# Optimization experiments

Measured on AMD Instinct MI355X. Metric: run time of the kernel, lower is better.

## Reference

```python
import jax, jax.numpy as jnp
import numpy as np

B, L, D_MODEL = 2, 4096, 256
D_STATE, D_CONV, EXPAND = 16, 4, 2
D_INNER = EXPAND * D_MODEL
DT_RANK = D_MODEL // 16
D_FF = 2048


def setup_inputs() -> dict:
    key = jax.random.key(0)
    ks = jax.random.split(key, 14)
    s = 0.02
    A_log = jnp.log(jnp.tile(jnp.arange(1, D_STATE + 1, dtype=jnp.float32), (D_INNER, 1)))
    return {
        "x": jax.random.normal(ks[0], (B, L, D_MODEL), jnp.float32),
        "in_proj_w": jax.random.normal(ks[1], (2 * D_INNER, D_MODEL), jnp.float32) * s,
        "conv_w": jax.random.normal(ks[2], (D_INNER, D_CONV), jnp.float32) * s,
        "conv_b": jax.random.normal(ks[3], (D_INNER,), jnp.float32) * s,
        "x_proj_w": jax.random.normal(ks[4], (DT_RANK + 2 * D_STATE, D_INNER), jnp.float32) * s,
        "dt_proj_w": jax.random.normal(ks[5], (D_INNER, DT_RANK), jnp.float32) * s,
        "dt_proj_b": jax.random.uniform(ks[6], (D_INNER,), jnp.float32, -4.0, -2.0),
        "A_log": A_log,
        "D": jnp.ones((D_INNER,), jnp.float32),
        "out_proj_w": jax.random.normal(ks[7], (D_MODEL, D_INNER), jnp.float32) * s,
        "lin1_w": jax.random.normal(ks[8], (D_FF, D_MODEL), jnp.float32) * s,
        "lin1_b": jnp.zeros((D_FF,), jnp.float32),
        "lin2_w": jax.random.normal(ks[9], (D_FF, D_FF), jnp.float32) * s,
        "lin2_b": jnp.zeros((D_FF,), jnp.float32),
    }


def reference(x, in_proj_w, conv_w, conv_b, x_proj_w, dt_proj_w, dt_proj_b,
              A_log, D, out_proj_w, lin1_w, lin1_b, lin2_w, lin2_b):
    b, l, _ = x.shape
    d_inner = conv_w.shape[0]
    d_state = A_log.shape[1]
    dt_rank = dt_proj_w.shape[1]
    d_conv = conv_w.shape[1]

    # in_proj -> split into x and gate z
    xz = x @ in_proj_w.T                       # (B,L,2*Din)
    xin, z = jnp.split(xz, 2, axis=-1)

    # causal depthwise conv1d + SiLU
    xc = jnp.transpose(xin, (0, 2, 1))         # (B,Din,L)
    xc = jax.lax.conv_general_dilated(
        xc, conv_w[:, None, :], (1,), [(d_conv - 1, 0)],
        dimension_numbers=("NCH", "OIH", "NCH"), feature_group_count=d_inner)
    xc = xc + conv_b[None, :, None]
    u = jax.nn.silu(jnp.transpose(xc, (0, 2, 1)))  # (B,L,Din)

    # input-dependent SSM params
    x_dbl = u @ x_proj_w.T                     # (B,L,dt_rank+2*N)
    dt, Bt, Ct = jnp.split(x_dbl, [dt_rank, dt_rank + d_state], axis=-1)
    delta = jax.nn.softplus(dt @ dt_proj_w.T + dt_proj_b)  # (B,L,Din)

    A = -jnp.exp(A_log)                        # (Din,N)
    dA = jnp.exp(delta[..., None] * A)         # (B,L,Din,N)
    dBu = delta[..., None] * Bt[:, :, None, :] * u[..., None]  # (B,L,Din,N)

    def step(h, inp):
        dA_t, dBu_t, C_t = inp
        h = dA_t * h + dBu_t                   # (B,Din,N)
        y = jnp.einsum("bdn,bn->bd", h, C_t)
        return h, y

    h0 = jnp.zeros((b, d_inner, d_state), x.dtype)
    _, ys = jax.lax.scan(step, h0, (jnp.swapaxes(dA, 0, 1),
                                    jnp.swapaxes(dBu, 0, 1),
                                    jnp.swapaxes(Ct, 0, 1)))
    y = jnp.swapaxes(ys, 0, 1) + u * D         # (B,L,Din)
    y = y * jax.nn.silu(z)
    m = y @ out_proj_w.T                       # (B,L,d_model)

    # trailing MLP: lin2(relu(lin1(.)))
    h1 = jax.nn.relu(m @ lin1_w.T + lin1_b)
    return h1 @ lin2_w.T + lin2_b
```

## Files before the change

kernel.cpp:

```cpp
#include <hip/hip_runtime.h>
#include <hip/hip_bf16.h>
#include <stdint.h>

#define BB  2
#define LL  4096
#define DM  256
#define DI  512
#define NST 16
#define DTR 16
#define DFF 2048
#define ML  (BB*LL)

#define NCHUNK 128
#define CHUNK  32
#define BDN    (BB*DI*NST)

typedef __attribute__((ext_vector_type(8))) short s16x8;
typedef __attribute__((ext_vector_type(4))) float f32x4;

__device__ __forceinline__ ushort f2bf(float f) {
  union { float f; uint32_t u; } v; v.f = f;
  return (ushort)((v.u + 0x7FFFu + ((v.u >> 16) & 1u)) >> 16);
}

__device__ __forceinline__ void async16(const void* g, void* l) {
  __builtin_amdgcn_global_load_lds(
      (const __attribute__((address_space(1))) void*)g,
      (__attribute__((address_space(3))) void*)l, 16, 0, 0);
}

__global__ void k_f2b(const float* __restrict__ src, ushort* __restrict__ dst, int n4) {
  int i = blockIdx.x * 256 + threadIdx.x;
  if (i >= n4) return;
  f32x4 v = ((const f32x4*)src)[i];
  *(ushort4*)&dst[i * 4] = make_ushort4(f2bf(v[0]), f2bf(v[1]), f2bf(v[2]), f2bf(v[3]));
}

__global__ void k_xprojw(const float* __restrict__ src, ushort* __restrict__ dst) {
  int i = blockIdx.x * 256 + threadIdx.x;
  if (i >= 128 * DI / 4) return;
  int e = i * 4;
  int r = e >> 9;
  int c = e & 511;
  ushort4 o;
  if (r < DTR + 2 * NST) {
    f32x4 v = *(const f32x4*)&src[r * DI + c];
    o = make_ushort4(f2bf(v[0]), f2bf(v[1]), f2bf(v[2]), f2bf(v[3]));
  } else {
    o = make_ushort4(0, 0, 0, 0);
  }
  *(ushort4*)&dst[e] = o;
}

template<int OUTF, int OUTB, int BIAS, int RELU>
__global__ __launch_bounds__(256)
void k_gemm(const ushort* __restrict__ A, const ushort* __restrict__ W,
            const float* __restrict__ bias,
            float* __restrict__ outF, ushort* __restrict__ outB,
            int M, int N, int K) {
  __shared__ __align__(16) ushort AsB[3][128 * 32];
  __shared__ __align__(16) ushort BsB[3][128 * 32];
  const int tid  = threadIdx.x;
  const int lane = tid & 63;
  const int wv   = tid >> 6;

  const int nwg  = gridDim.x * gridDim.y;
  const int flat = blockIdx.y * gridDim.x + blockIdx.x;
  const int cpx  = nwg >> 3;
  const int swz  = (flat & 7) * cpx + (flat >> 3);
  const int m0 = (swz / gridDim.x) << 7;
  const int n0 = (swz % gridDim.x) << 7;

  const int wr = (wv >> 1) << 6;
  const int wc = (wv & 1) << 6;
  const int lr = lane & 15;
  const int hi = lane >> 4;

  f32x4 acc[4][4] = {};

  const int sr0 = (wv << 5) + (lane >> 2);
  const int sc  = lane & 3;

  const int nt = K >> 5;

  auto STAGE = [&](int t, int bi) {
    const int k0 = t << 5;
#pragma unroll
    for (int j = 0; j < 2; ++j) {
      const int r  = sr0 + j * 16;
      const int cs = sc ^ ((r >> 1) & 3);
      async16(A + (size_t)(m0 + r) * K + k0 + cs * 8, &AsB[bi][((wv << 5) + j * 16) * 32]);
      async16(W + (size_t)(n0 + r) * K + k0 + cs * 8, &BsB[bi][((wv << 5) + j * 16) * 32]);
    }
  };

  STAGE(0, 0);
  STAGE(1, 1);

  int cur = 0;
  for (int t = 0; t < nt; ++t) {
    if (t + 1 < nt) { asm volatile("s_waitcnt vmcnt(4)" ::: "memory"); }
    else            { asm volatile("s_waitcnt vmcnt(0)" ::: "memory"); }
    __builtin_amdgcn_s_barrier();
    __builtin_amdgcn_sched_barrier(0);

    if (t + 2 < nt) {
      int nx2 = cur + 2; if (nx2 >= 3) nx2 -= 3;
      STAGE(t + 2, nx2);
    }

    const ushort* As = AsB[cur];
    const ushort* Bs = BsB[cur];
    s16x8 af[4], bf_[4];
#pragma unroll
    for (int mi = 0; mi < 4; ++mi) {
      const int row = wr + mi * 16 + lr;
      af[mi] = *(const s16x8*)&As[row * 32 + ((hi ^ ((row >> 1) & 3)) << 3)];
    }
#pragma unroll
    for (int ni = 0; ni < 4; ++ni) {
      const int row = wc + ni * 16 + lr;
      bf_[ni] = *(const s16x8*)&Bs[row * 32 + ((hi ^ ((row >> 1) & 3)) << 3)];
    }
    asm volatile("s_waitcnt lgkmcnt(0)" ::: "memory");
    __builtin_amdgcn_sched_barrier(0);

    __builtin_amdgcn_s_setprio(1);
#pragma unroll
    for (int mi = 0; mi < 4; ++mi)
#pragma unroll
      for (int ni = 0; ni < 4; ++ni)
        acc[mi][ni] = __builtin_amdgcn_mfma_f32_16x16x32_bf16(af[mi], bf_[ni], acc[mi][ni], 0, 0, 0);
    __builtin_amdgcn_s_setprio(0);

    cur = (cur + 1 == 3) ? 0 : cur + 1;
  }

#pragma unroll
  for (int mi = 0; mi < 4; ++mi) {
#pragma unroll
    for (int ni = 0; ni < 4; ++ni) {
      const int gc = n0 + wc + ni * 16 + lr;
      const float b = BIAS ? bias[gc] : 0.f;
#pragma unroll
      for (int i = 0; i < 4; ++i) {
        const int gr = m0 + wr + mi * 16 + (hi << 2) + i;
        float v = acc[mi][ni][i] + b;
        if (RELU) v = fmaxf(v, 0.f);
        if (OUTF) outF[(size_t)gr * N + gc] = v;
        if (OUTB) outB[(size_t)gr * N + gc] = f2bf(v);
      }
    }
  }
}

__global__ void k_conv(const float* __restrict__ xz, const float* __restrict__ cw,
                       const float* __restrict__ cb,
                       float* __restrict__ u, ushort* __restrict__ u_bf) {
  const int i = blockIdx.x * 256 + threadIdx.x;
  if (i >= ML * DI / 4) return;
  const int d4 = i & (DI / 4 - 1);
  const int bl = i / (DI / 4);
  const int l  = bl & (LL - 1);
  const int d  = d4 << 2;
  f32x4 acc;
  acc[0] = cb[d]; acc[1] = cb[d + 1]; acc[2] = cb[d + 2]; acc[3] = cb[d + 3];
#pragma unroll
  for (int j = 0; j < 4; ++j) {
    const int lj = l - 3 + j;
    if (lj >= 0) {
      const f32x4 xv = *(const f32x4*)&xz[(size_t)(bl + j - 3) * 1024 + d];
      acc[0] += xv[0] * cw[(d + 0) * 4 + j];
      acc[1] += xv[1] * cw[(d + 1) * 4 + j];
      acc[2] += xv[2] * cw[(d + 2) * 4 + j];
      acc[3] += xv[3] * cw[(d + 3) * 4 + j];
    }
  }
  f32x4 o;
#pragma unroll
  for (int c = 0; c < 4; ++c) o[c] = acc[c] / (1.f + __expf(-acc[c]));
  *(f32x4*)&u[(size_t)bl * DI + d] = o;
  *(ushort4*)&u_bf[(size_t)bl * DI + d] =
      make_ushort4(f2bf(o[0]), f2bf(o[1]), f2bf(o[2]), f2bf(o[3]));
}

__global__ __launch_bounds__(256)
void k_scan1(const float* __restrict__ u, const float* __restrict__ xdbl,
             const float* __restrict__ A_log, const float* __restrict__ dtw,
             const float* __restrict__ dtb,
             float* __restrict__ Pw, float* __restrict__ Sw) {
  const int c = blockIdx.x;
  const int b = blockIdx.y >> 1;
  const int d = ((blockIdx.y & 1) << 8) + threadIdx.x;
  __shared__ float sdt[CHUNK][16], sB[CHUNK][16];
  {
    const int i = threadIdx.x * 2;
    const int t = i >> 4, n = i & 15;
    const size_t g = ((size_t)b * LL + (size_t)c * CHUNK + t) * 128 + n;
    *(float2*)&sdt[t][n] = *(const float2*)&xdbl[g];
    *(float2*)&sB[t][n]  = *(const float2*)&xdbl[g + DTR];
  }
  float An[16], wreg[16];
#pragma unroll
  for (int j = 0; j < 4; ++j) {
    f32x4 a = *(const f32x4*)&A_log[d * 16 + j * 4];
    f32x4 w = *(const f32x4*)&dtw[d * 16 + j * 4];
#pragma unroll
    for (int q = 0; q < 4; ++q) { An[j * 4 + q] = -__expf(a[q]); wreg[j * 4 + q] = w[q]; }
  }
  const float bd = dtb[d];
  float P[16], S[16];
#pragma unroll
  for (int n = 0; n < 16; ++n) { P[n] = 1.f; S[n] = 0.f; }
  __syncthreads();

  const size_t rowbase = ((size_t)b * LL + (size_t)c * CHUNK) * DI + d;
  float ut = u[rowbase];
  for (int t = 0; t < CHUNK; ++t) {
    const float ut_n = (t + 1 < CHUNK) ? u[rowbase + (size_t)(t + 1) * DI] : 0.f;
    float a = bd;
#pragma unroll
    for (int k2 = 0; k2 < 16; ++k2) a = fmaf(sdt[t][k2], wreg[k2], a);
    const float dt = (a > 15.f) ? a : log1pf(__expf(a));
    const float k = dt * ut;
#pragma unroll
    for (int n = 0; n < 16; ++n) {
      const float dA = __expf(dt * An[n]);
      S[n] = fmaf(dA, S[n], k * sB[t][n]);
      P[n] *= dA;
    }
    ut = ut_n;
  }
  float* Pp = Pw + ((size_t)c * BDN) + ((size_t)b * DI + d) * 16;
  float* Sp = Sw + ((size_t)c * BDN) + ((size_t)b * DI + d) * 16;
#pragma unroll
  for (int j = 0; j < 4; ++j) {
    f32x4 pv, sv;
#pragma unroll
    for (int q = 0; q < 4; ++q) { pv[q] = P[j * 4 + q]; sv[q] = S[j * 4 + q]; }
    *(f32x4*)&Pp[j * 4] = pv;
    *(f32x4*)&Sp[j * 4] = sv;
  }
}

__global__ void k_scan2(float* __restrict__ Pw, const float* __restrict__ Sw) {
  const int f = blockIdx.x * 256 + threadIdx.x;
  float h = 0.f;
#pragma unroll 4
  for (int c = 0; c < NCHUNK; ++c) {
    const float Pc = Pw[(size_t)c * BDN + f];
    const float Sc = Sw[(size_t)c * BDN + f];
    Pw[(size_t)c * BDN + f] = h;
    h = fmaf(Pc, h, Sc);
  }
}

__global__ __launch_bounds__(256)
void k_scan3(const float* __restrict__ u, const float* __restrict__ xdbl,
             const float* __restrict__ xz, const float* __restrict__ A_log,
             const float* __restrict__ dtw, const float* __restrict__ dtb,
             const float* __restrict__ Dp,
             const float* __restrict__ Hs, ushort* __restrict__ y_bf) {
  const int c = blockIdx.x;
  const int b = blockIdx.y >> 1;
  const int d = ((blockIdx.y & 1) << 8) + threadIdx.x;
  __shared__ float sdt[CHUNK][16], sB[CHUNK][16], sC[CHUNK][16];
  {
    const int i = threadIdx.x * 2;
    const int t = i >> 4, n = i & 15;
    const size_t g = ((size_t)b * LL + (size_t)c * CHUNK + t) * 128 + n;
    *(float2*)&sdt[t][n] = *(const float2*)&xdbl[g];
    *(float2*)&sB[t][n]  = *(const float2*)&xdbl[g + DTR];
    *(float2*)&sC[t][n]  = *(const float2*)&xdbl[g + DTR + NST];
  }
  float An[16], wreg[16];
#pragma unroll
  for (int j = 0; j < 4; ++j) {
    f32x4 a = *(const f32x4*)&A_log[d * 16 + j * 4];
    f32x4 w = *(const f32x4*)&dtw[d * 16 + j * 4];
#pragma unroll
    for (int q = 0; q < 4; ++q) { An[j * 4 + q] = -__expf(a[q]); wreg[j * 4 + q] = w[q]; }
  }
  const float bd = dtb[d];
  float h[16];
  {
    const float* Hp = Hs + ((size_t)c * BDN) + ((size_t)b * DI + d) * 16;
#pragma unroll
    for (int j = 0; j < 4; ++j) {
      f32x4 v = *(const f32x4*)&Hp[j * 4];
#pragma unroll
      for (int q = 0; q < 4; ++q) h[j * 4 + q] = v[q];
    }
  }
  const float Dd = Dp[d];
  __syncthreads();

  const size_t rowbase = ((size_t)b * LL + (size_t)c * CHUNK) * DI + d;
  const size_t zbase   = ((size_t)b * LL + (size_t)c * CHUNK) * 1024 + DI + d;
  float ut = u[rowbase];
  float zt = xz[zbase];
  for (int t = 0; t < CHUNK; ++t) {
    float ut_n = 0.f, zt_n = 0.f;
    if (t + 1 < CHUNK) {
      ut_n = u[rowbase + (size_t)(t + 1) * DI];
      zt_n = xz[zbase + (size_t)(t + 1) * 1024];
    }
    float a = bd;
#pragma unroll
    for (int k2 = 0; k2 < 16; ++k2) a = fmaf(sdt[t][k2], wreg[k2], a);
    const float dt = (a > 15.f) ? a : log1pf(__expf(a));
    const float k = dt * ut;
    float y = 0.f;
#pragma unroll
    for (int n = 0; n < 16; ++n) {
      const float dA = __expf(dt * An[n]);
      h[n] = fmaf(dA, h[n], k * sB[t][n]);
      y = fmaf(h[n], sC[t][n], y);
    }
    y = (y + ut * Dd) * (zt / (1.f + __expf(-zt)));
    y_bf[rowbase + (size_t)t * DI] = f2bf(y);
    ut = ut_n; zt = zt_n;
  }
}

extern "C" void kernel_launch(void* const* d_in, const int* in_sizes, int n_in,
                              void* d_out, int out_size, void* d_ws, size_t ws_size,
                              hipStream_t stream) {
  const float* x          = (const float*)d_in[0];
  const float* in_proj_w  = (const float*)d_in[1];
  const float* conv_w     = (const float*)d_in[2];
  const float* conv_b     = (const float*)d_in[3];
  const float* x_proj_w   = (const float*)d_in[4];
  const float* dt_proj_w  = (const float*)d_in[5];
  const float* dt_proj_b  = (const float*)d_in[6];
  const float* A_log      = (const float*)d_in[7];
  const float* Dp         = (const float*)d_in[8];
  const float* out_proj_w = (const float*)d_in[9];
  const float* lin1_w     = (const float*)d_in[10];
  const float* lin1_b     = (const float*)d_in[11];
  const float* lin2_w     = (const float*)d_in[12];
  const float* lin2_b     = (const float*)d_in[13];
  float* out = (float*)d_out;

  char* p = (char*)d_ws;
  auto carve = [&](size_t bytes) -> char* {
    char* r = p;
    p += (bytes + 255) & ~(size_t)255;
    return r;
  };
  ushort* x_bf   = (ushort*)carve((size_t)ML * DM * 2);
  ushort* wip_bf = (ushort*)carve((size_t)2 * DI * DM * 2);
  float*  xz     = (float*) carve((size_t)ML * 1024 * 4);
  float*  u      = (float*) carve((size_t)ML * DI * 4);
  ushort* u_bf   = (ushort*)carve((size_t)ML * DI * 2);
  ushort* xpw_bf = (ushort*)carve((size_t)128 * DI * 2);
  float*  xdbl   = (float*) carve((size_t)ML * 128 * 4);
  ushort* y_bf   = (ushort*)carve((size_t)ML * DI * 2);
  ushort* opw_bf = (ushort*)carve((size_t)DM * DI * 2);
  ushort* l1w_bf = (ushort*)carve((size_t)DFF * DM * 2);
  float*  Pws    = (float*) carve((size_t)NCHUNK * BDN * 4);
  float*  Sws    = (float*) carve((size_t)NCHUNK * BDN * 4);
  ushort* m_bf   = u_bf;
  ushort* h1_bf  = (ushort*)xz;
  ushort* l2w_bf = (ushort*)u;

  k_f2b<<<(ML * DM / 4 + 255) / 256, 256, 0, stream>>>(x, x_bf, ML * DM / 4);
  k_f2b<<<(2 * DI * DM / 4 + 255) / 256, 256, 0, stream>>>(in_proj_w, wip_bf, 2 * DI * DM / 4);
  k_gemm<1, 0, 0, 0><<<dim3(1024 / 128, ML / 128), 256, 0, stream>>>(
      x_bf, wip_bf, nullptr, xz, nullptr, ML, 1024, DM);
  k_conv<<<(ML * DI / 4 + 255) / 256, 256, 0, stream>>>(xz, conv_w, conv_b, u, u_bf);
  k_xprojw<<<(128 * DI / 4 + 255) / 256, 256, 0, stream>>>(x_proj_w, xpw_bf);
  k_gemm<1, 0, 0, 0><<<dim3(1, ML / 128), 256, 0, stream>>>(
      u_bf, xpw_bf, nullptr, xdbl, nullptr, ML, 128, DI);
  k_scan1<<<dim3(NCHUNK, BB * 2), 256, 0, stream>>>(u, xdbl, A_log, dt_proj_w,
                                                    dt_proj_b, Pws, Sws);
  k_scan2<<<BDN / 256, 256, 0, stream>>>(Pws, Sws);
  k_scan3<<<dim3(NCHUNK, BB * 2), 256, 0, stream>>>(u, xdbl, xz, A_log, dt_proj_w,
                                                    dt_proj_b, Dp, Pws, y_bf);
  k_f2b<<<(DM * DI / 4 + 255) / 256, 256, 0, stream>>>(out_proj_w, opw_bf, DM * DI / 4);
  k_gemm<0, 1, 0, 0><<<dim3(DM / 128, ML / 128), 256, 0, stream>>>(
      y_bf, opw_bf, nullptr, nullptr, m_bf, ML, DM, DI);
  k_f2b<<<(DFF * DM / 4 + 255) / 256, 256, 0, stream>>>(lin1_w, l1w_bf, DFF * DM / 4);
  k_gemm<0, 1, 1, 1><<<dim3(DFF / 128, ML / 128), 256, 0, stream>>>(
      m_bf, l1w_bf, lin1_b, nullptr, h1_bf, ML, DFF, DM);
  k_f2b<<<(DFF * DFF / 4 + 255) / 256, 256, 0, stream>>>(lin2_w, l2w_bf, DFF * DFF / 4);
  k_gemm<1, 0, 1, 0><<<dim3(DFF / 128, ML / 128), 256, 0, stream>>>(
      h1_bf, l2w_bf, lin2_b, out, nullptr, ML, DFF, DFF);
}
```

Baseline: 378.3 us.

## Add 256x256-tile 8-wave GEMM with 4-stage pipeline for MLP layers

```diff
diff --git a/kernel.cpp b/kernel.cpp
--- a/kernel.cpp
+++ b/kernel.cpp
@@ -67,7 +67,7 @@
   const int nwg  = gridDim.x * gridDim.y;
   const int flat = blockIdx.y * gridDim.x + blockIdx.x;
   const int cpx  = nwg >> 3;
-  const int swz  = (flat & 7) * cpx + (flat >> 3);
+  const int swz  = (nwg & 7) ? flat : (flat & 7) * cpx + (flat >> 3);
   const int m0 = (swz / gridDim.x) << 7;
   const int n0 = (swz % gridDim.x) << 7;
 
@@ -80,7 +80,6 @@
 
   const int sr0 = (wv << 5) + (lane >> 2);
   const int sc  = lane & 3;
-
   const int nt = K >> 5;
 
   auto STAGE = [&](int t, int bi) {
@@ -145,6 +144,107 @@
 #pragma unroll
       for (int i = 0; i < 4; ++i) {
         const int gr = m0 + wr + mi * 16 + (hi << 2) + i;
+        float v = acc[mi][ni][i] + b;
+        if (RELU) v = fmaxf(v, 0.f);
+        if (OUTF) outF[(size_t)gr * N + gc] = v;
+        if (OUTB) outB[(size_t)gr * N + gc] = f2bf(v);
+      }
+    }
+  }
+}
+
+template<int OUTF, int OUTB, int BIAS, int RELU>
+__global__ __launch_bounds__(512, 2)
+void k_gemm256(const ushort* __restrict__ A, const ushort* __restrict__ W,
+               const float* __restrict__ bias,
+               float* __restrict__ outF, ushort* __restrict__ outB,
+               int M, int N, int K) {
+  __shared__ __align__(16) ushort AsB[4][256 * 32];
+  __shared__ __align__(16) ushort BsB[4][256 * 32];
+  const int tid  = threadIdx.x;
+  const int lane = tid & 63;
+  const int wv   = tid >> 6;
+
+  const int nwg  = gridDim.x * gridDim.y;
+  const int flat = blockIdx.y * gridDim.x + blockIdx.x;
+  const int cpx  = nwg >> 3;
+  const int swz  = (nwg & 7) ? flat : (flat & 7) * cpx + (flat >> 3);
+  const int m0 = (swz / gridDim.x) << 8;
+  const int n0 = (swz % gridDim.x) << 8;
+
+  const int wrM = (wv >> 2) << 7;
+  const int wcN = (wv & 3) << 6;
+  const int lr = lane & 15;
+  const int hi = lane >> 4;
+
+  f32x4 acc[8][4] = {};
+
+  const int sr0 = (wv << 5) + (lane >> 2);
+  const int sc  = lane & 3;
+  const int nt  = K >> 5;
+
+  auto STAGE = [&](int t, int bi) {
+    const int k0 = t << 5;
+#pragma unroll
+    for (int j = 0; j < 2; ++j) {
+      const int r  = sr0 + j * 16;
+      const int cs = sc ^ ((r >> 1) & 3);
+      async16(A + (size_t)(m0 + r) * K + k0 + cs * 8, &AsB[bi][((wv << 5) + j * 16) * 32]);
+      async16(W + (size_t)(n0 + r) * K + k0 + cs * 8, &BsB[bi][((wv << 5) + j * 16) * 32]);
+    }
+  };
+
+  STAGE(0, 0);
+  STAGE(1, 1);
+  STAGE(2, 2);
+
+  int cur = 0;
+  for (int t = 0; t < nt; ++t) {
+    const int fly = nt - 1 - t;
+    if (fly >= 2)      { asm volatile("s_waitcnt vmcnt(8)" ::: "memory"); }
+    else if (fly == 1) { asm volatile("s_waitcnt vmcnt(4)" ::: "memory"); }
+    else               { asm volatile("s_waitcnt vmcnt(0)" ::: "memory"); }
+    __builtin_amdgcn_s_barrier();
+    __builtin_amdgcn_sched_barrier(0);
+
+    if (t + 3 < nt) STAGE(t + 3, (cur + 3) & 3);
+
+    const ushort* As = AsB[cur];
+    const ushort* Bs = BsB[cur];
+    s16x8 bf_[4], af[8];
+#pragma unroll
+    for (int ni = 0; ni < 4; ++ni) {
+      const int row = wcN + ni * 16 + lr;
+      bf_[ni] = *(const s16x8*)&Bs[row * 32 + ((hi ^ ((row >> 1) & 3)) << 3)];
+    }
+#pragma unroll
+    for (int mi = 0; mi < 8; ++mi) {
+      const int row = wrM + mi * 16 + lr;
+      af[mi] = *(const s16x8*)&As[row * 32 + ((hi ^ ((row >> 1) & 3)) << 3)];
+    }
+    asm volatile("s_waitcnt lgkmcnt(0)" ::: "memory");
+    __builtin_amdgcn_sched_barrier(0);
+
+    __builtin_amdgcn_s_setprio(1);
+#pragma unroll
+    for (int mi = 0; mi < 8; ++mi)
+#pragma unroll
+      for (int ni = 0; ni < 4; ++ni)
+        acc[mi][ni] = __builtin_amdgcn_mfma_f32_16x16x32_bf16(af[mi], bf_[ni], acc[mi][ni], 0, 0, 0);
+    __builtin_amdgcn_s_setprio(0);
+
+    cur = (cur + 1) & 3;
+  }
+
+#pragma unroll
+  for (int mi = 0; mi < 8; ++mi) {
+#pragma unroll
+    for (int ni = 0; ni < 4; ++ni) {
+      const int gc = n0 + wcN + ni * 16 + lr;
+      const float b = BIAS ? bias[gc] : 0.f;
+#pragma unroll
+      for (int i = 0; i < 4; ++i) {
+        const int gr = m0 + wrM + mi * 16 + (hi << 2) + i;
         float v = acc[mi][ni][i] + b;
         if (RELU) v = fmaxf(v, 0.f);
         if (OUTF) outF[(size_t)gr * N + gc] = v;
@@ -381,9 +481,9 @@
   k_gemm<0, 1, 0, 0><<<dim3(DM / 128, ML / 128), 256, 0, stream>>>(
       y_bf, opw_bf, nullptr, nullptr, m_bf, ML, DM, DI);
   k_f2b<<<(DFF * DM / 4 + 255) / 256, 256, 0, stream>>>(lin1_w, l1w_bf, DFF * DM / 4);
-  k_gemm<0, 1, 1, 1><<<dim3(DFF / 128, ML / 128), 256, 0, stream>>>(
+  k_gemm256<0, 1, 1, 1><<<dim3(DFF / 256, ML / 256), 512, 0, stream>>>(
       m_bf, l1w_bf, lin1_b, nullptr, h1_bf, ML, DFF, DM);
   k_f2b<<<(DFF * DFF / 4 + 255) / 256, 256, 0, stream>>>(lin2_w, l2w_bf, DFF * DFF / 4);
-  k_gemm<1, 0, 1, 0><<<dim3(DFF / 128, ML / 128), 256, 0, stream>>>(
+  k_gemm256<1, 0, 1, 0><<<dim3(DFF / 256, ML / 256), 512, 0, stream>>>(
       h1_bf, l2w_bf, lin2_b, out, nullptr, ML, DFF, DFF);
 }
```

After: 369.5 us. 2.3% less time.
